# Kernel tuning notes

Measured on AMD Instinct MI355X. Metric: run time of the kernel, lower is better.

## Reference

```python
import jax, jax.numpy as jnp
import numpy as np

T, B, D = 512, 64, 1024

def setup_inputs() -> dict:
    key = jax.random.key(0)
    ks = jax.random.split(key, 4)
    s = 1.0 / np.sqrt(D)
    return {
        "x": jax.random.normal(ks[0], (T, B, D), dtype=jnp.float32),
        "W_ih": jax.random.normal(ks[1], (4 * D, D), dtype=jnp.float32) * s,
        "W_hh": jax.random.normal(ks[2], (4 * D, D), dtype=jnp.float32) * s,
        "b_ih": jnp.zeros((4 * D,), dtype=jnp.float32),
        "b_hh": jnp.zeros((4 * D,), dtype=jnp.float32),
        "W_proj": jax.random.normal(ks[3], (2, D), dtype=jnp.float32) * s,
        "b_proj": jnp.zeros((2,), dtype=jnp.float32),
    }

def reference(x, W_ih, W_hh, b_ih, b_hh, W_proj, b_proj):
    d = x.shape[-1]
    bsz = x.shape[1]
    h0 = jnp.zeros((bsz, d), dtype=x.dtype)
    c0 = jnp.zeros((bsz, d), dtype=x.dtype)

    def cell(carry, x_t):
        h, c = carry
        # torch.nn.LSTMCell gate math, gate order i, f, g, o
        gates = x_t @ W_ih.T + b_ih + h @ W_hh.T + b_hh  # [B, 4D]
        i, f, g, o = jnp.split(gates, 4, axis=-1)
        i = jax.nn.sigmoid(i)
        f = jax.nn.sigmoid(f)
        g = jnp.tanh(g)
        o = jax.nn.sigmoid(o)
        c_new = f * c + i * g
        h_new = o * jnp.tanh(c_new)
        return (h_new, c_new), None

    (h_final, _), _ = jax.lax.scan(cell, (h0, c0), x)
    logit = jax.nn.log_softmax(h_final @ W_proj.T + b_proj, axis=-1)  # [B, 2]
    return logit
```

## Files before the change

### kernel.cpp

```cpp
#include <hip/hip_runtime.h>


typedef float f32x4 __attribute__((ext_vector_type(4)));
typedef short bf16x8 __attribute__((ext_vector_type(8)));
typedef unsigned long long u64;

#define T_STEPS 512

__device__ inline unsigned short f2bf(float f) {
  unsigned u = __float_as_uint(f);
  u = u + 0x7FFFu + ((u >> 16) & 1u);
  return (unsigned short)(u >> 16);
}
__device__ inline float bf2f(unsigned short s) {
  return __uint_as_float(((unsigned)s) << 16);
}
__device__ inline float sigf(float x) { return 1.f / (1.f + __expf(-x)); }
__device__ inline float tanh_f(float x) {
  float e = __expf(-2.f * fabsf(x));
  float r = (1.f - e) / (1.f + e);
  return x >= 0.f ? r : -r;
}

__device__ inline bf16x8 load_h16_sc1(const unsigned short* p) {
  bf16x8 r;
  asm volatile("global_load_dwordx4 %0, %1, off sc1"
               : "=v"(r)
               : "v"((u64)p));
  return r;
}

__global__ void convert_x(const float* __restrict__ x,
                          unsigned short* __restrict__ Xb, int n4) {
  int i = blockIdx.x * blockDim.x + threadIdx.x;
  const int stride = gridDim.x * blockDim.x;
  for (; i < n4; i += stride) {
    float4 v = ((const float4*)x)[i];
    ushort4 o;
    o.x = f2bf(v.x); o.y = f2bf(v.y); o.z = f2bf(v.z); o.w = f2bf(v.w);
    ((ushort4*)Xb)[i] = o;
  }
}

__global__ void permute_w(const float* __restrict__ Wih,
                          const float* __restrict__ Whh,
                          const float* __restrict__ bih,
                          const float* __restrict__ bhh,
                          unsigned short* __restrict__ WihP,
                          unsigned short* __restrict__ WhhP,
                          float* __restrict__ biasP) {
  const int p = blockIdx.x;
  const int i = p >> 4, u = (p >> 2) & 3, g = p & 3;
  const int orig = g * 1024 + i * 4 + u;
  const int k = threadIdx.x * 4;
  float4 a = *(const float4*)(Wih + (size_t)orig * 1024 + k);
  ushort4 oa; oa.x = f2bf(a.x); oa.y = f2bf(a.y); oa.z = f2bf(a.z); oa.w = f2bf(a.w);
  *(ushort4*)(WihP + (size_t)p * 1024 + k) = oa;
  float4 b = *(const float4*)(Whh + (size_t)orig * 1024 + k);
  ushort4 ob; ob.x = f2bf(b.x); ob.y = f2bf(b.y); ob.z = f2bf(b.z); ob.w = f2bf(b.w);
  *(ushort4*)(WhhP + (size_t)p * 1024 + k) = ob;
  if (threadIdx.x == 0) biasP[p] = bih[orig] + bhh[orig];
}

__global__ __launch_bounds__(256, 2) void gemm_ih(
    const unsigned short* __restrict__ Xb,
    const unsigned short* __restrict__ WihP,
    const float* __restrict__ biasP,
    unsigned short* __restrict__ G) {
  __shared__ unsigned short Alds[128 * 64];
  __shared__ unsigned short Blds[128 * 64];
  const int tid = threadIdx.x, lane = tid & 63, wave = tid >> 6;
  const int mt = blockIdx.y, nt = blockIdx.x;
  const int wm = (wave >> 1) * 64, wn = (wave & 1) * 64;

  f32x4 acc[4][4];
  {
    f32x4 z = {0.f, 0.f, 0.f, 0.f};
#pragma unroll
    for (int m = 0; m < 4; ++m)
#pragma unroll
      for (int n = 0; n < 4; ++n) acc[m][n] = z;
  }

  const int srow = lane >> 3;
  const int schunk = (lane & 7) ^ srow;
  const int frow = lane & 15;
  const int kgrp = lane >> 4;

  for (int kt = 0; kt < 16; ++kt) {
    __syncthreads();
#pragma unroll
    for (int q = 0; q < 4; ++q) {
      const int rr = (wave * 4 + q) * 8 + srow;
      const unsigned short* ga =
          Xb + (size_t)(mt * 128 + rr) * 1024 + kt * 64 + schunk * 8;
      __builtin_amdgcn_global_load_lds(
          (const __attribute__((address_space(1))) void*)ga,
          (__attribute__((address_space(3))) void*)(Alds + (wave * 4 + q) * 512),
          16, 0, 0);
      const unsigned short* gb =
          WihP + (size_t)(nt * 128 + rr) * 1024 + kt * 64 + schunk * 8;
      __builtin_amdgcn_global_load_lds(
          (const __attribute__((address_space(1))) void*)gb,
          (__attribute__((address_space(3))) void*)(Blds + (wave * 4 + q) * 512),
          16, 0, 0);
    }
    __syncthreads();
#pragma unroll
    for (int kk = 0; kk < 2; ++kk) {
      bf16x8 av[4], bv[4];
      const int kb = kk * 32 + 8 * kgrp;
#pragma unroll
      for (int i = 0; i < 4; ++i) {
        const int ra = wm + 16 * i + frow;
        av[i] = *(const bf16x8*)(Alds + ra * 64 + (kb ^ ((ra & 7) << 3)));
        const int rb = wn + 16 * i + frow;
        bv[i] = *(const bf16x8*)(Blds + rb * 64 + (kb ^ ((rb & 7) << 3)));
      }
#pragma unroll
      for (int m = 0; m < 4; ++m)
#pragma unroll
        for (int n = 0; n < 4; ++n)
          acc[m][n] = __builtin_amdgcn_mfma_f32_16x16x32_bf16(
              av[m], bv[n], acc[m][n], 0, 0, 0);
    }
  }
#pragma unroll
  for (int n = 0; n < 4; ++n) {
    const int col = nt * 128 + wn + 16 * n + frow;
    const float bvv = biasP[col];
#pragma unroll
    for (int m = 0; m < 4; ++m) {
      const int row0 = mt * 128 + wm + 16 * m + kgrp * 4;
#pragma unroll
      for (int r = 0; r < 4; ++r)
        __builtin_nontemporal_store(
            f2bf(acc[m][n][r] + bvv),
            G + (size_t)(row0 + r) * 4096 + col);
    }
  }
}

__global__ __launch_bounds__(256, 1) void lstm_grouped(
    const unsigned short* __restrict__ G,
    const unsigned short* __restrict__ WhhP,
    unsigned short* __restrict__ hbuf,
    float* __restrict__ hfinal,
    const float* __restrict__ Wproj, const float* __restrict__ bproj,
    float* __restrict__ out,
    unsigned short* __restrict__ flags) {
  __shared__ unsigned short Wlds[64 * 1024];
  __shared__ float Gbuf[4][16][68];
  const int tid = threadIdx.x, lane = tid & 63, wave = tid >> 6;
  const int bid = blockIdx.x;
  const int p = bid >> 6, c = bid & 63;

  {
    const int r = tid >> 2, q = tid & 3;
    const unsigned short* src = WhhP + (size_t)(c * 64 + r) * 1024 + q * 256;
    unsigned short* dstb = Wlds + r * 1024;
    const int swz = (r & 7) << 3;
#pragma unroll
    for (int j = 0; j < 256; j += 8) {
      uint4 v = *(const uint4*)(src + j);
      *(uint4*)(dstb + ((q * 256 + j) ^ swz)) = v;
    }
  }

  const int ub = tid >> 4, uu = tid & 15;
  const int lpb = 16 * (uu >> 2) + 4 * (uu & 3);
  const int frow = lane & 15, kgrp = lane >> 4;
  const int wbase = wave * 256;
  const u64* fq = (const u64*)(flags + p * 64) + (lane & 15);

  const int hrd_base =
      wave * 4096 + (kgrp >> 1) * 256 + frow * 16 + (kgrp & 1) * 8;

  float c_state = 0.f;
  ushort4 gcur;
  {
    union { u64 q; ushort4 v; } ug;
    ug.q = __builtin_nontemporal_load(
        (const u64*)(G + (size_t)(p * 16 + ub) * 4096 + c * 64 + lpb));
    gcur = ug.v;
  }
  __syncthreads();

  for (int t = 0; t < T_STEPS; ++t) {
    const unsigned short* hread = hbuf + (size_t)(t & 1) * 65536 + p * 16384;
    unsigned short* hwrite =
        hbuf + (size_t)((t + 1) & 1) * 65536 + p * 16384;

    ushort4 gnext = gcur;
    if (t + 1 < T_STEPS) {
      union { u64 q; ushort4 v; } ug;
      ug.q = __builtin_nontemporal_load(
          (const u64*)(G + (size_t)((t + 1) * 64 + p * 16 + ub) * 4096 +
                       c * 64 + lpb));
      gnext = ug.v;
    }

    if (wave == 0 && lane < 16) {
      unsigned guard = 0;
      while (true) {
        u64 q = __hip_atomic_load(fq, __ATOMIC_RELAXED,
                                  __HIP_MEMORY_SCOPE_AGENT);
        unsigned m0 = (unsigned)(q & 0xFFFFu);
        unsigned m1 = (unsigned)((q >> 16) & 0xFFFFu);
        unsigned m2 = (unsigned)((q >> 32) & 0xFFFFu);
        unsigned m3 = (unsigned)((q >> 48) & 0xFFFFu);
        unsigned mn = min(min(m0, m1), min(m2, m3));
        if (__all(mn >= (unsigned)t)) break;
        __builtin_amdgcn_s_sleep(1);
        if (++guard > (1u << 22)) break;
      }
    }
    __syncthreads();

    f32x4 acc[4];
    {
      f32x4 z = {0.f, 0.f, 0.f, 0.f};
      acc[0] = z; acc[1] = z; acc[2] = z; acc[3] = z;
    }
    bf16x8 av[8];
    {
      const unsigned short* abase = hread + hrd_base;
#pragma unroll
      for (int kw = 0; kw < 8; ++kw)
        av[kw] = load_h16_sc1(abase + kw * 512);
    }
    asm volatile("s_waitcnt vmcnt(0)" ::: "memory");
    __builtin_amdgcn_sched_barrier(0);

#pragma unroll
    for (int kw = 0; kw < 8; ++kw) {
      const int k = wbase + kw * 32 + 8 * kgrp;
#pragma unroll
      for (int n = 0; n < 4; ++n) {
        const int pcol = n * 16 + frow;
        bf16x8 bv =
            *(const bf16x8*)(Wlds + pcol * 1024 + (k ^ ((pcol & 7) << 3)));
        acc[n] = __builtin_amdgcn_mfma_f32_16x16x32_bf16(av[kw], bv, acc[n],
                                                         0, 0, 0);
      }
    }

    {
      float* gp = &Gbuf[wave][0][0];
#pragma unroll
      for (int n = 0; n < 4; ++n)
#pragma unroll
        for (int r = 0; r < 4; ++r)
          gp[(4 * kgrp + r) * 68 + n * 16 + frow] = acc[n][r];
    }
    __syncthreads();

    {
      f32x4 g4 = *(const f32x4*)(&Gbuf[0][ub][lpb]);
#pragma unroll
      for (int w = 1; w < 4; ++w) {
        f32x4 gw = *(const f32x4*)(&Gbuf[w][ub][lpb]);
        g4.x += gw.x; g4.y += gw.y; g4.z += gw.z; g4.w += gw.w;
      }
      const unsigned short* gc = (const unsigned short*)&gcur;
      const float ig = sigf(g4.x + bf2f(gc[0]));
      const float fg = sigf(g4.y + bf2f(gc[1]));
      const float gg = tanh_f(g4.z + bf2f(gc[2]));
      const float og = sigf(g4.w + bf2f(gc[3]));
      c_state = fg * c_state + ig * gg;
      const float hv = og * tanh_f(c_state);
      const unsigned hb = (unsigned)f2bf(hv);
      const unsigned b1 = (unsigned)__shfl_down((int)hb, 1);
      const unsigned b2 = (unsigned)__shfl_down((int)hb, 2);
      const unsigned b3 = (unsigned)__shfl_down((int)hb, 3);
      if (t == T_STEPS - 1)
        __hip_atomic_store(
            (unsigned*)(hfinal + (size_t)(p * 16 + ub) * 1024 + c * 16 + uu),
            __float_as_uint(hv), __ATOMIC_RELAXED, __HIP_MEMORY_SCOPE_AGENT);
      if ((uu & 3) == 0) {
        const u64 pk = (u64)(hb | (b1 << 16)) | ((u64)(b2 | (b3 << 16)) << 32);
        __hip_atomic_store((u64*)(hwrite + c * 256 + ub * 16 + uu), pk,
                           __ATOMIC_RELAXED, __HIP_MEMORY_SCOPE_AGENT);
      }
      gcur = gnext;
    }
    asm volatile("s_waitcnt vmcnt(0)" ::: "memory");
    __syncthreads();
    if (tid == 0)
      __hip_atomic_store(flags + p * 64 + c, (unsigned short)(t + 1),
                         __ATOMIC_RELAXED, __HIP_MEMORY_SCOPE_AGENT);
  }

  if (c == 0) {
    if (wave == 0 && lane < 16) {
      unsigned guard = 0;
      while (true) {
        u64 q = __hip_atomic_load(fq, __ATOMIC_RELAXED,
                                  __HIP_MEMORY_SCOPE_AGENT);
        unsigned m0 = (unsigned)(q & 0xFFFFu);
        unsigned m1 = (unsigned)((q >> 16) & 0xFFFFu);
        unsigned m2 = (unsigned)((q >> 32) & 0xFFFFu);
        unsigned m3 = (unsigned)((q >> 48) & 0xFFFFu);
        unsigned mn = min(min(m0, m1), min(m2, m3));
        if (__all(mn >= (unsigned)T_STEPS)) break;
        __builtin_amdgcn_s_sleep(1);
        if (++guard > (1u << 22)) break;
      }
    }
    __syncthreads();
    const int b = tid >> 4, seg = tid & 15;
    const float* hf = hfinal + (size_t)(p * 16 + b) * 1024 + seg * 64;
    const float* w0 = Wproj + seg * 64;
    const float* w1 = Wproj + 1024 + seg * 64;
    float s0 = 0.f, s1 = 0.f;
    for (int k = 0; k < 64; k += 2) {
      u64 hq = __hip_atomic_load((const u64*)(hf + k), __ATOMIC_RELAXED,
                                 __HIP_MEMORY_SCOPE_AGENT);
      union { u64 q; float f[2]; } uh;
      uh.q = hq;
      float2 wv0 = *(const float2*)(w0 + k);
      float2 wv1 = *(const float2*)(w1 + k);
      s0 += uh.f[0] * wv0.x + uh.f[1] * wv0.y;
      s1 += uh.f[0] * wv1.x + uh.f[1] * wv1.y;
    }
#pragma unroll
    for (int off = 8; off > 0; off >>= 1) {
      s0 += __shfl_down(s0, off, 16);
      s1 += __shfl_down(s1, off, 16);
    }
    if (seg == 0) {
      s0 += bproj[0];
      s1 += bproj[1];
      const float mx = fmaxf(s0, s1);
      const float lse = mx + logf(expf(s0 - mx) + expf(s1 - mx));
      out[(p * 16 + b) * 2 + 0] = s0 - lse;
      out[(p * 16 + b) * 2 + 1] = s1 - lse;
    }
  }
}

extern "C" void kernel_launch(void* const* d_in, const int* in_sizes, int n_in,
                              void* d_out, int out_size, void* d_ws,
                              size_t ws_size, hipStream_t stream) {
  const float* x = (const float*)d_in[0];
  const float* Wih = (const float*)d_in[1];
  const float* Whh = (const float*)d_in[2];
  const float* bih = (const float*)d_in[3];
  const float* bhh = (const float*)d_in[4];
  const float* Wproj = (const float*)d_in[5];
  const float* bproj = (const float*)d_in[6];
  float* out = (float*)d_out;

  const size_t OFF_G = 0;
  const size_t OFF_XB = 268435456;
  const size_t OFF_WIH = 335544320;
  const size_t OFF_WHH = 343932928;
  const size_t OFF_BIAS = 352321536;
  const size_t OFF_H = 352337920;
  const size_t OFF_HF = 352600064;
  const size_t OFF_SYNC = 352862208;
  const size_t TOTAL = 352866304;

  if (ws_size < TOTAL) {
    (void)hipMemsetAsync(d_out, 0, (size_t)out_size * sizeof(float), stream);
    return;
  }
  char* ws = (char*)d_ws;
  unsigned short* G = (unsigned short*)(ws + OFF_G);
  unsigned short* Xb = (unsigned short*)(ws + OFF_XB);
  unsigned short* WihP = (unsigned short*)(ws + OFF_WIH);
  unsigned short* WhhP = (unsigned short*)(ws + OFF_WHH);
  float* biasP = (float*)(ws + OFF_BIAS);
  unsigned short* hbuf = (unsigned short*)(ws + OFF_H);
  float* hfinal = (float*)(ws + OFF_HF);
  unsigned short* flags = (unsigned short*)(ws + OFF_SYNC);

  (void)hipMemsetAsync(hbuf, 0, 262144, stream);
  (void)hipMemsetAsync(flags, 0, 4096, stream);

  convert_x<<<2048, 256, 0, stream>>>(x, Xb, 512 * 64 * 1024 / 4);
  permute_w<<<4096, 256, 0, stream>>>(Wih, Whh, bih, bhh, WihP, WhhP, biasP);
  gemm_ih<<<dim3(32, 256), 256, 0, stream>>>(Xb, WihP, biasP, G);
  lstm_grouped<<<256, 256, 0, stream>>>(G, WhhP, hbuf, hfinal, Wproj, bproj,
                                        out, flags);
}
```

Before: 2.269 ms.

## Embed step counters in hidden-state words to replace flag-based inter-block sync

Each hidden-state store now carries two bf16 values plus a 32-bit timestep tag. Consumers poll the data loads themselves until every tag matches the current step, so the separate per-step flag polling, the extra barrier, and the vmcnt wait before publishing a flag are all removed. This takes one global round trip and one barrier off the critical path of every recurrent step. In exchange, the h exchange buffer doubles in size and each poll reloads the full h tile, which adds memory traffic while blocks wait.

Measured after the change: 2.336 ms. +2.9%, slower.

```diff
diff --git a/kernel.cpp b/kernel.cpp
--- a/kernel.cpp
+++ b/kernel.cpp
@@ -22,8 +22,8 @@
   return x >= 0.f ? r : -r;
 }
 
-__device__ inline bf16x8 load_h16_sc1(const unsigned short* p) {
-  bf16x8 r;
+__device__ inline uint4 load16_sc1(const void* p) {
+  uint4 r;
   asm volatile("global_load_dwordx4 %0, %1, off sc1"
                : "=v"(r)
                : "v"((u64)p));
@@ -144,7 +144,7 @@
 __global__ __launch_bounds__(256, 1) void lstm_grouped(
     const unsigned short* __restrict__ G,
     const unsigned short* __restrict__ WhhP,
-    unsigned short* __restrict__ hbuf,
+    u64* __restrict__ hx,
     float* __restrict__ hfinal,
     const float* __restrict__ Wproj, const float* __restrict__ bproj,
     float* __restrict__ out,
@@ -171,10 +171,15 @@
   const int lpb = 16 * (uu >> 2) + 4 * (uu & 3);
   const int frow = lane & 15, kgrp = lane >> 4;
   const int wbase = wave * 256;
-  const u64* fq = (const u64*)(flags + p * 64) + (lane & 15);
-
-  const int hrd_base =
-      wave * 4096 + (kgrp >> 1) * 256 + frow * 16 + (kgrp & 1) * 8;
+
+  int ridx[8];
+#pragma unroll
+  for (int kw = 0; kw < 8; ++kw) {
+    const int U = wbase + kw * 32 + kgrp * 8;
+    ridx[kw] = ((U >> 4) << 7) + frow * 8 + ((U >> 1) & 4);
+  }
+
+  u64* const hxg = hx + (size_t)p * 8192;
 
   float c_state = 0.f;
   ushort4 gcur;
@@ -187,9 +192,8 @@
   __syncthreads();
 
   for (int t = 0; t < T_STEPS; ++t) {
-    const unsigned short* hread = hbuf + (size_t)(t & 1) * 65536 + p * 16384;
-    unsigned short* hwrite =
-        hbuf + (size_t)((t + 1) & 1) * 65536 + p * 16384;
+    const u64* rbase = hxg + (size_t)(t & 1) * 32768;
+    u64* wnext = hxg + (size_t)((t + 1) & 1) * 32768;
 
     ushort4 gnext = gcur;
     if (t + 1 < T_STEPS) {
@@ -200,6 +204,99 @@
       gnext = ug.v;
     }
 
+    uint4 rec[16];
+    {
+      const unsigned want = (unsigned)t;
+      unsigned guard = 0;
+      while (true) {
+#pragma unroll
+        for (int kw = 0; kw < 8; ++kw) {
+          rec[2 * kw] = load16_sc1(rbase + ridx[kw]);
+          rec[2 * kw + 1] = load16_sc1(rbase + ridx[kw] + 2);
+        }
+        asm volatile("s_waitcnt vmcnt(0)" ::: "memory");
+        __builtin_amdgcn_sched_barrier(0);
+        bool good = true;
+#pragma unroll
+        for (int i = 0; i < 16; ++i)
+          good = good && (rec[i].y == want) && (rec[i].w == want);
+        if (__all(good)) break;
+        __builtin_amdgcn_s_sleep(1);
+        if (++guard > (1u << 20)) break;
+      }
+    }
+
+    f32x4 acc[4];
+    {
+      f32x4 z = {0.f, 0.f, 0.f, 0.f};
+      acc[0] = z; acc[1] = z; acc[2] = z; acc[3] = z;
+    }
+#pragma unroll
+    for (int kw = 0; kw < 8; ++kw) {
+      union { unsigned w[4]; bf16x8 v; } ua;
+      ua.w[0] = rec[2 * kw].x;
+      ua.w[1] = rec[2 * kw].z;
+      ua.w[2] = rec[2 * kw + 1].x;
+      ua.w[3] = rec[2 * kw + 1].z;
+      const int k = wbase + kw * 32 + 8 * kgrp;
+#pragma unroll
+      for (int n = 0; n < 4; ++n) {
+        const int pcol = n * 16 + frow;
+        bf16x8 bv =
+            *(const bf16x8*)(Wlds + pcol * 1024 + (k ^ ((pcol & 7) << 3)));
+        acc[n] = __builtin_amdgcn_mfma_f32_16x16x32_bf16(ua.v, bv, acc[n],
+                                                         0, 0, 0);
+      }
+    }
+
+    {
+      float* gp = &Gbuf[wave][0][0];
+#pragma unroll
+      for (int n = 0; n < 4; ++n)
+#pragma unroll
+        for (int r = 0; r < 4; ++r)
+          gp[(4 * kgrp + r) * 68 + n * 16 + frow] = acc[n][r];
+    }
+    __syncthreads();
+
+    {
+      f32x4 g4 = *(const f32x4*)(&Gbuf[0][ub][lpb]);
+#pragma unroll
+      for (int w = 1; w < 4; ++w) {
+        f32x4 gw = *(const f32x4*)(&Gbuf[w][ub][lpb]);
+        g4.x += gw.x; g4.y += gw.y; g4.z += gw.z; g4.w += gw.w;
+      }
+      const unsigned short* gc = (const unsigned short*)&gcur;
+      const float ig = sigf(g4.x + bf2f(gc[0]));
+      const float fg = sigf(g4.y + bf2f(gc[1]));
+      const float gg = tanh_f(g4.z + bf2f(gc[2]));
+      const float og = sigf(g4.w + bf2f(gc[3]));
+      c_state = fg * c_state + ig * gg;
+      const float hv = og * tanh_f(c_state);
+      const unsigned hb = (unsigned)f2bf(hv);
+      const unsigned nb = (unsigned)__shfl_down((int)hb, 1);
+      if (t == T_STEPS - 1)
+        __hip_atomic_store(
+            (unsigned*)(hfinal + (size_t)(p * 16 + ub) * 1024 + c * 16 + uu),
+            __float_as_uint(hv), __ATOMIC_RELAXED, __HIP_MEMORY_SCOPE_AGENT);
+      if ((tid & 1) == 0) {
+        const u64 pk = (u64)(hb | (nb << 16)) | ((u64)(unsigned)(t + 1) << 32);
+        __hip_atomic_store(wnext + (c * 128 + (tid >> 1)), pk,
+                           __ATOMIC_RELAXED, __HIP_MEMORY_SCOPE_AGENT);
+      }
+      gcur = gnext;
+    }
+    __syncthreads();
+  }
+
+  asm volatile("s_waitcnt vmcnt(0)" ::: "memory");
+  __syncthreads();
+  if (tid == 0)
+    __hip_atomic_store(flags + p * 64 + c, (unsigned short)1,
+                       __ATOMIC_RELAXED, __HIP_MEMORY_SCOPE_AGENT);
+
+  if (c == 0) {
+    const u64* fq = (const u64*)(flags + p * 64) + (lane & 15);
     if (wave == 0 && lane < 16) {
       unsigned guard = 0;
       while (true) {
@@ -210,99 +307,7 @@
         unsigned m2 = (unsigned)((q >> 32) & 0xFFFFu);
         unsigned m3 = (unsigned)((q >> 48) & 0xFFFFu);
         unsigned mn = min(min(m0, m1), min(m2, m3));
-        if (__all(mn >= (unsigned)t)) break;
-        __builtin_amdgcn_s_sleep(1);
-        if (++guard > (1u << 22)) break;
-      }
-    }
-    __syncthreads();
-
-    f32x4 acc[4];
-    {
-      f32x4 z = {0.f, 0.f, 0.f, 0.f};
-      acc[0] = z; acc[1] = z; acc[2] = z; acc[3] = z;
-    }
-    bf16x8 av[8];
-    {
-      const unsigned short* abase = hread + hrd_base;
-#pragma unroll
-      for (int kw = 0; kw < 8; ++kw)
-        av[kw] = load_h16_sc1(abase + kw * 512);
-    }
-    asm volatile("s_waitcnt vmcnt(0)" ::: "memory");
-    __builtin_amdgcn_sched_barrier(0);
-
-#pragma unroll
-    for (int kw = 0; kw < 8; ++kw) {
-      const int k = wbase + kw * 32 + 8 * kgrp;
-#pragma unroll
-      for (int n = 0; n < 4; ++n) {
-        const int pcol = n * 16 + frow;
-        bf16x8 bv =
-            *(const bf16x8*)(Wlds + pcol * 1024 + (k ^ ((pcol & 7) << 3)));
-        acc[n] = __builtin_amdgcn_mfma_f32_16x16x32_bf16(av[kw], bv, acc[n],
-                                                         0, 0, 0);
-      }
-    }
-
-    {
-      float* gp = &Gbuf[wave][0][0];
-#pragma unroll
-      for (int n = 0; n < 4; ++n)
-#pragma unroll
-        for (int r = 0; r < 4; ++r)
-          gp[(4 * kgrp + r) * 68 + n * 16 + frow] = acc[n][r];
-    }
-    __syncthreads();
-
-    {
-      f32x4 g4 = *(const f32x4*)(&Gbuf[0][ub][lpb]);
-#pragma unroll
-      for (int w = 1; w < 4; ++w) {
-        f32x4 gw = *(const f32x4*)(&Gbuf[w][ub][lpb]);
-        g4.x += gw.x; g4.y += gw.y; g4.z += gw.z; g4.w += gw.w;
-      }
-      const unsigned short* gc = (const unsigned short*)&gcur;
-      const float ig = sigf(g4.x + bf2f(gc[0]));
-      const float fg = sigf(g4.y + bf2f(gc[1]));
-      const float gg = tanh_f(g4.z + bf2f(gc[2]));
-      const float og = sigf(g4.w + bf2f(gc[3]));
-      c_state = fg * c_state + ig * gg;
-      const float hv = og * tanh_f(c_state);
-      const unsigned hb = (unsigned)f2bf(hv);
-      const unsigned b1 = (unsigned)__shfl_down((int)hb, 1);
-      const unsigned b2 = (unsigned)__shfl_down((int)hb, 2);
-      const unsigned b3 = (unsigned)__shfl_down((int)hb, 3);
-      if (t == T_STEPS - 1)
-        __hip_atomic_store(
-            (unsigned*)(hfinal + (size_t)(p * 16 + ub) * 1024 + c * 16 + uu),
-            __float_as_uint(hv), __ATOMIC_RELAXED, __HIP_MEMORY_SCOPE_AGENT);
-      if ((uu & 3) == 0) {
-        const u64 pk = (u64)(hb | (b1 << 16)) | ((u64)(b2 | (b3 << 16)) << 32);
-        __hip_atomic_store((u64*)(hwrite + c * 256 + ub * 16 + uu), pk,
-                           __ATOMIC_RELAXED, __HIP_MEMORY_SCOPE_AGENT);
-      }
-      gcur = gnext;
-    }
-    asm volatile("s_waitcnt vmcnt(0)" ::: "memory");
-    __syncthreads();
-    if (tid == 0)
-      __hip_atomic_store(flags + p * 64 + c, (unsigned short)(t + 1),
-                         __ATOMIC_RELAXED, __HIP_MEMORY_SCOPE_AGENT);
-  }
-
-  if (c == 0) {
-    if (wave == 0 && lane < 16) {
-      unsigned guard = 0;
-      while (true) {
-        u64 q = __hip_atomic_load(fq, __ATOMIC_RELAXED,
-                                  __HIP_MEMORY_SCOPE_AGENT);
-        unsigned m0 = (unsigned)(q & 0xFFFFu);
-        unsigned m1 = (unsigned)((q >> 16) & 0xFFFFu);
-        unsigned m2 = (unsigned)((q >> 32) & 0xFFFFu);
-        unsigned m3 = (unsigned)((q >> 48) & 0xFFFFu);
-        unsigned mn = min(min(m0, m1), min(m2, m3));
-        if (__all(mn >= (unsigned)T_STEPS)) break;
+        if (__all(mn >= 1u)) break;
         __builtin_amdgcn_s_sleep(1);
         if (++guard > (1u << 22)) break;
       }
@@ -356,10 +361,10 @@
   const size_t OFF_WIH = 335544320;
   const size_t OFF_WHH = 343932928;
   const size_t OFF_BIAS = 352321536;
-  const size_t OFF_H = 352337920;
-  const size_t OFF_HF = 352600064;
-  const size_t OFF_SYNC = 352862208;
-  const size_t TOTAL = 352866304;
+  const size_t OFF_HX = 352337920;
+  const size_t OFF_HF = 352862208;
+  const size_t OFF_SYNC = 353124352;
+  const size_t TOTAL = 353128448;
 
   if (ws_size < TOTAL) {
     (void)hipMemsetAsync(d_out, 0, (size_t)out_size * sizeof(float), stream);
@@ -371,16 +376,16 @@
   unsigned short* WihP = (unsigned short*)(ws + OFF_WIH);
   unsigned short* WhhP = (unsigned short*)(ws + OFF_WHH);
   float* biasP = (float*)(ws + OFF_BIAS);
-  unsigned short* hbuf = (unsigned short*)(ws + OFF_H);
+  u64* hx = (u64*)(ws + OFF_HX);
   float* hfinal = (float*)(ws + OFF_HF);
   unsigned short* flags = (unsigned short*)(ws + OFF_SYNC);
 
-  (void)hipMemsetAsync(hbuf, 0, 262144, stream);
+  (void)hipMemsetAsync(hx, 0, 524288, stream);
   (void)hipMemsetAsync(flags, 0, 4096, stream);
 
   convert_x<<<2048, 256, 0, stream>>>(x, Xb, 512 * 64 * 1024 / 4);
   permute_w<<<4096, 256, 0, stream>>>(Wih, Whh, bih, bhh, WihP, WhhP, biasP);
   gemm_ih<<<dim3(32, 256), 256, 0, stream>>>(Xb, WihP, biasP, G);
-  lstm_grouped<<<256, 256, 0, stream>>>(G, WhhP, hbuf, hfinal, Wproj, bproj,
+  lstm_grouped<<<256, 256, 0, stream>>>(G, WhhP, hx, hfinal, Wproj, bproj,
                                         out, flags);
 }
```

## Hold W_hh slices in registers with 128 blocks of 512 threads

Applied to the files above, without the earlier changes.

The recurrent kernel now runs as 128 blocks of 512 threads, each owning 128 gate columns. Each wave keeps its W_hh slice in VGPRs (32 bf16x8 fragments) rather than staging 128KB in LDS, which removes the per-step LDS reads of weights. Halving the block count also halves the number of participants in the per-step cross-block flag synchronization. The cost is heavy register pressure, an 8-way LDS reduction of partial sums, and a changed h-buffer layout that has to match what the readers expect.

Measured after the change: 2.720 ms. +19.8%, slower.

```diff
diff --git a/kernel.cpp b/kernel.cpp
--- a/kernel.cpp
+++ b/kernel.cpp
@@ -141,7 +141,7 @@
   }
 }
 
-__global__ __launch_bounds__(256, 1) void lstm_grouped(
+__global__ __launch_bounds__(512, 2) void lstm_grouped(
     const unsigned short* __restrict__ G,
     const unsigned short* __restrict__ WhhP,
     unsigned short* __restrict__ hbuf,
@@ -149,39 +149,35 @@
     const float* __restrict__ Wproj, const float* __restrict__ bproj,
     float* __restrict__ out,
     unsigned short* __restrict__ flags) {
-  __shared__ unsigned short Wlds[64 * 1024];
-  __shared__ float Gbuf[4][16][68];
+  __shared__ float Gbuf[8][16][164];
   const int tid = threadIdx.x, lane = tid & 63, wave = tid >> 6;
   const int bid = blockIdx.x;
-  const int p = bid >> 6, c = bid & 63;
-
-  {
-    const int r = tid >> 2, q = tid & 3;
-    const unsigned short* src = WhhP + (size_t)(c * 64 + r) * 1024 + q * 256;
-    unsigned short* dstb = Wlds + r * 1024;
-    const int swz = (r & 7) << 3;
-#pragma unroll
-    for (int j = 0; j < 256; j += 8) {
-      uint4 v = *(const uint4*)(src + j);
-      *(uint4*)(dstb + ((q * 256 + j) ^ swz)) = v;
-    }
-  }
-
-  const int ub = tid >> 4, uu = tid & 15;
-  const int lpb = 16 * (uu >> 2) + 4 * (uu & 3);
+  const int p = bid >> 5, c = bid & 31;
+
+  const int ub = tid >> 5;
+  const int lu = tid & 31;
+  const int lpb = 16 * (lu >> 2) + 4 * (lu & 3);
   const int frow = lane & 15, kgrp = lane >> 4;
-  const int wbase = wave * 256;
-  const u64* fq = (const u64*)(flags + p * 64) + (lane & 15);
-
-  const int hrd_base =
-      wave * 4096 + (kgrp >> 1) * 256 + frow * 16 + (kgrp & 1) * 8;
+  const int wbase = wave * 128;
+
+  bf16x8 wreg[4][8];
+#pragma unroll
+  for (int kw = 0; kw < 4; ++kw)
+#pragma unroll
+    for (int n = 0; n < 8; ++n)
+      wreg[kw][n] = *(const bf16x8*)(
+          WhhP + (size_t)(c * 128 + n * 16 + frow) * 1024 + wbase + kw * 32 +
+          8 * kgrp);
+
+  const u64* fq = (const u64*)(flags + p * 32) + (lane & 7);
+  const int hrd_base = wave * 2048 + frow * 32 + 8 * kgrp;
 
   float c_state = 0.f;
   ushort4 gcur;
   {
     union { u64 q; ushort4 v; } ug;
     ug.q = __builtin_nontemporal_load(
-        (const u64*)(G + (size_t)(p * 16 + ub) * 4096 + c * 64 + lpb));
+        (const u64*)(G + (size_t)(p * 16 + ub) * 4096 + c * 128 + lpb));
     gcur = ug.v;
   }
   __syncthreads();
@@ -196,11 +192,11 @@
       union { u64 q; ushort4 v; } ug;
       ug.q = __builtin_nontemporal_load(
           (const u64*)(G + (size_t)((t + 1) * 64 + p * 16 + ub) * 4096 +
-                       c * 64 + lpb));
+                       c * 128 + lpb));
       gnext = ug.v;
     }
 
-    if (wave == 0 && lane < 16) {
+    if (wave == 0 && lane < 8) {
       unsigned guard = 0;
       while (true) {
         u64 q = __hip_atomic_load(fq, __ATOMIC_RELAXED,
@@ -217,48 +213,43 @@
     }
     __syncthreads();
 
-    f32x4 acc[4];
+    bf16x8 av[4];
+    {
+      const unsigned short* abase = hread + hrd_base;
+#pragma unroll
+      for (int kw = 0; kw < 4; ++kw)
+        av[kw] = load_h16_sc1(abase + kw * 512);
+    }
+    asm volatile("s_waitcnt vmcnt(0)" ::: "memory");
+    __builtin_amdgcn_sched_barrier(0);
+
+    f32x4 acc[8];
     {
       f32x4 z = {0.f, 0.f, 0.f, 0.f};
-      acc[0] = z; acc[1] = z; acc[2] = z; acc[3] = z;
-    }
-    bf16x8 av[8];
-    {
-      const unsigned short* abase = hread + hrd_base;
-#pragma unroll
-      for (int kw = 0; kw < 8; ++kw)
-        av[kw] = load_h16_sc1(abase + kw * 512);
-    }
-    asm volatile("s_waitcnt vmcnt(0)" ::: "memory");
-    __builtin_amdgcn_sched_barrier(0);
-
-#pragma unroll
-    for (int kw = 0; kw < 8; ++kw) {
-      const int k = wbase + kw * 32 + 8 * kgrp;
-#pragma unroll
-      for (int n = 0; n < 4; ++n) {
-        const int pcol = n * 16 + frow;
-        bf16x8 bv =
-            *(const bf16x8*)(Wlds + pcol * 1024 + (k ^ ((pcol & 7) << 3)));
-        acc[n] = __builtin_amdgcn_mfma_f32_16x16x32_bf16(av[kw], bv, acc[n],
-                                                         0, 0, 0);
-      }
-    }
+#pragma unroll
+      for (int n = 0; n < 8; ++n) acc[n] = z;
+    }
+#pragma unroll
+    for (int kw = 0; kw < 4; ++kw)
+#pragma unroll
+      for (int n = 0; n < 8; ++n)
+        acc[n] = __builtin_amdgcn_mfma_f32_16x16x32_bf16(av[kw], wreg[kw][n],
+                                                         acc[n], 0, 0, 0);
 
     {
       float* gp = &Gbuf[wave][0][0];
 #pragma unroll
-      for (int n = 0; n < 4; ++n)
+      for (int n = 0; n < 8; ++n)
 #pragma unroll
         for (int r = 0; r < 4; ++r)
-          gp[(4 * kgrp + r) * 68 + n * 16 + frow] = acc[n][r];
+          gp[(4 * kgrp + r) * 164 + n * 16 + frow] = acc[n][r];
     }
     __syncthreads();
 
     {
       f32x4 g4 = *(const f32x4*)(&Gbuf[0][ub][lpb]);
 #pragma unroll
-      for (int w = 1; w < 4; ++w) {
+      for (int w = 1; w < 8; ++w) {
         f32x4 gw = *(const f32x4*)(&Gbuf[w][ub][lpb]);
         g4.x += gw.x; g4.y += gw.y; g4.z += gw.z; g4.w += gw.w;
       }
@@ -275,11 +266,11 @@
       const unsigned b3 = (unsigned)__shfl_down((int)hb, 3);
       if (t == T_STEPS - 1)
         __hip_atomic_store(
-            (unsigned*)(hfinal + (size_t)(p * 16 + ub) * 1024 + c * 16 + uu),
+            (unsigned*)(hfinal + (size_t)(p * 16 + ub) * 1024 + c * 32 + lu),
             __float_as_uint(hv), __ATOMIC_RELAXED, __HIP_MEMORY_SCOPE_AGENT);
-      if ((uu & 3) == 0) {
+      if ((lu & 3) == 0) {
         const u64 pk = (u64)(hb | (b1 << 16)) | ((u64)(b2 | (b3 << 16)) << 32);
-        __hip_atomic_store((u64*)(hwrite + c * 256 + ub * 16 + uu), pk,
+        __hip_atomic_store((u64*)(hwrite + c * 512 + ub * 32 + lu), pk,
                            __ATOMIC_RELAXED, __HIP_MEMORY_SCOPE_AGENT);
       }
       gcur = gnext;
@@ -287,12 +278,12 @@
     asm volatile("s_waitcnt vmcnt(0)" ::: "memory");
     __syncthreads();
     if (tid == 0)
-      __hip_atomic_store(flags + p * 64 + c, (unsigned short)(t + 1),
+      __hip_atomic_store(flags + p * 32 + c, (unsigned short)(t + 1),
                          __ATOMIC_RELAXED, __HIP_MEMORY_SCOPE_AGENT);
   }
 
   if (c == 0) {
-    if (wave == 0 && lane < 16) {
+    if (wave == 0 && lane < 8) {
       unsigned guard = 0;
       while (true) {
         u64 q = __hip_atomic_load(fq, __ATOMIC_RELAXED,
@@ -308,12 +299,12 @@
       }
     }
     __syncthreads();
-    const int b = tid >> 4, seg = tid & 15;
-    const float* hf = hfinal + (size_t)(p * 16 + b) * 1024 + seg * 64;
-    const float* w0 = Wproj + seg * 64;
-    const float* w1 = Wproj + 1024 + seg * 64;
+    const int b = tid >> 5, seg = tid & 31;
+    const float* hf = hfinal + (size_t)(p * 16 + b) * 1024 + seg * 32;
+    const float* w0 = Wproj + seg * 32;
+    const float* w1 = Wproj + 1024 + seg * 32;
     float s0 = 0.f, s1 = 0.f;
-    for (int k = 0; k < 64; k += 2) {
+    for (int k = 0; k < 32; k += 2) {
       u64 hq = __hip_atomic_load((const u64*)(hf + k), __ATOMIC_RELAXED,
                                  __HIP_MEMORY_SCOPE_AGENT);
       union { u64 q; float f[2]; } uh;
@@ -324,9 +315,9 @@
       s1 += uh.f[0] * wv1.x + uh.f[1] * wv1.y;
     }
 #pragma unroll
-    for (int off = 8; off > 0; off >>= 1) {
-      s0 += __shfl_down(s0, off, 16);
-      s1 += __shfl_down(s1, off, 16);
+    for (int off = 16; off > 0; off >>= 1) {
+      s0 += __shfl_down(s0, off, 32);
+      s1 += __shfl_down(s1, off, 32);
     }
     if (seg == 0) {
       s0 += bproj[0];
@@ -381,6 +372,6 @@
   convert_x<<<2048, 256, 0, stream>>>(x, Xb, 512 * 64 * 1024 / 4);
   permute_w<<<4096, 256, 0, stream>>>(Wih, Whh, bih, bhh, WihP, WhhP, biasP);
   gemm_ih<<<dim3(32, 256), 256, 0, stream>>>(Xb, WihP, biasP, G);
-  lstm_grouped<<<256, 256, 0, stream>>>(G, WhhP, hbuf, hfinal, Wproj, bproj,
+  lstm_grouped<<<128, 512, 0, stream>>>(G, WhhP, hbuf, hfinal, Wproj, bproj,
                                         out, flags);
 }
```
